# Optimization experiments

Measured on AMD Instinct MI355X. Metric: run time of the kernel, lower is better.

The kernel has to match this reference:

```python
import jax, jax.numpy as jnp
import numpy as np
from jax import lax

E = 8          # num_experts
C = 768        # n_embd
H = 3072       # expert_hidden_dim
TOP_K = 2
TEMPERATURE = 1.0


def setup_inputs() -> dict:
    key = jax.random.key(0)
    ks = jax.random.split(key, 6)
    B, T = 4, 2048
    x = jax.random.normal(ks[0], (B, T, C), dtype=jnp.float32)
    # router: Linear(C, E, bias=False); store as [C, E] so logits = x @ Wr
    Wr = jax.random.normal(ks[1], (C, E), dtype=jnp.float32) / np.sqrt(C)
    # stacked expert params
    W1 = jax.random.normal(ks[2], (E, C, H), dtype=jnp.float32) / np.sqrt(C)
    b1 = jnp.zeros((E, H), dtype=jnp.float32)
    W2 = jax.random.normal(ks[3], (E, H, C), dtype=jnp.float32) / np.sqrt(H)
    b2 = jnp.zeros((E, C), dtype=jnp.float32)
    return {"x": x, "Wr": Wr, "W1": W1, "b1": b1, "W2": W2, "b2": b2}


def reference(x, Wr, W1, b1, W2, b2):
    B, T, Cdim = x.shape
    xf = x.reshape(-1, Cdim)                         # [N, C]
    logits = (xf @ Wr) / TEMPERATURE                 # [N, E]
    prob = jax.nn.softmax(logits, axis=-1)
    top_prob, top_idx = lax.top_k(prob, TOP_K)       # [N, k]
    top_prob = top_prob / (top_prob.sum(-1, keepdims=True) + 1e-9)
    onehot = jax.nn.one_hot(top_idx, E, dtype=xf.dtype)     # [N, k, E]
    # per-token weight for each expert (zero if not selected)
    weights = jnp.einsum('nke,nk->en', onehot, top_prob)    # [E, N]
    # token counts per expert (top_k indices are distinct, so any == sum)
    counts = onehot.max(axis=1).sum(axis=0)                  # [E]
    utilization = counts / (counts.sum() + 1e-9)

    def step(acc, ew):
        W1e, b1e, W2e, b2e, we = ew
        h = jax.nn.gelu(xf @ W1e + b1e, approximate=False)   # [N, H]
        y = h @ W2e + b2e                                     # [N, C]
        return acc + we[:, None] * y, None

    out_flat, _ = lax.scan(step, jnp.zeros_like(xf), (W1, b1, W2, b2, weights))
    return out_flat.reshape(B, T, Cdim), utilization
```

## Files before the change

kernel.cpp:

```cpp
#include <hip/hip_runtime.h>

typedef unsigned short u16;
typedef unsigned int u32;
typedef __bf16 bf16x8 __attribute__((ext_vector_type(8)));
typedef float f32x4 __attribute__((ext_vector_type(4)));

#define NTOK 8192
#define CDIM 768
#define HDIM 3072
#define NEXP 8
#define NPAIR 16384
#define HB 32

__device__ __forceinline__ float b2f(u16 u){ u32 v = ((u32)u)<<16; float f; __builtin_memcpy(&f,&v,4); return f; }
__device__ __forceinline__ u16 f2b(float f){ u32 u; __builtin_memcpy(&u,&f,4); u32 r = (u + 0x7FFF + ((u>>16)&1)) >> 16; return (u16)r; }
__device__ __forceinline__ int iclamp(int v,int lo,int hi){ return v<lo?lo:(v>hi?hi:v); }

__device__ __forceinline__ float gelu_f(float v){
  float x = fabsf(v)*0.70710678118654752f;
  float t = __builtin_amdgcn_rcpf(1.0f + 0.3275911f*x);
  float p = ((((1.061405429f*t - 1.453152027f)*t + 1.421413741f)*t - 0.284496736f)*t + 0.254829592f)*t;
  float er = 1.0f - p*__expf(-x*x);
  er = copysignf(er, v);
  return 0.5f*v*(1.0f+er);
}

__device__ __forceinline__ void gl2l16(const void* g, void* l){
  __builtin_amdgcn_global_load_lds((const __attribute__((address_space(1))) void*)g,
                                   (__attribute__((address_space(3))) void*)l, 16, 0, 0);
}

__global__ void detect_k(const u16* __restrict__ x, int* __restrict__ flagp){
  __shared__ int cnt;
  if (threadIdx.x==0) cnt=0;
  __syncthreads();
  int bad=0;
  for (int i=threadIdx.x; i<2048; i+=256){
    u16 u = x[i];
    int ex = (u>>7)&0xFF;
    if (ex >= 134) bad++;
  }
  if (bad) atomicAdd(&cnt, bad);
  __syncthreads();
  if (threadIdx.x==0) *flagp = (cnt > 32) ? 1 : 0;
}

__global__ __launch_bounds__(256) void conv_k(const void* __restrict__ src, u16* __restrict__ dst,
                                              int n4, const int* __restrict__ flagp){
  int i = blockIdx.x*256 + threadIdx.x;
  if (i >= n4) return;
  if (*flagp){
    float4 v = ((const float4*)src)[i];
    ushort4 o; o.x=f2b(v.x); o.y=f2b(v.y); o.z=f2b(v.z); o.w=f2b(v.w);
    ((ushort4*)dst)[i] = o;
  } else {
    ((ushort4*)dst)[i] = ((const ushort4*)src)[i];
  }
}

__global__ __launch_bounds__(256) void router_k(const void* __restrict__ xraw, const void* __restrict__ Wrraw,
    const int* __restrict__ flagp,
    int* __restrict__ tok_e, float* __restrict__ tok_w){
  int fp32f = *flagp;
  int tok = blockIdx.x*4 + (threadIdx.x>>6);
  int lane = threadIdx.x & 63;
  double acc[8];
  #pragma unroll
  for(int e=0;e<8;e++) acc[e]=0.0;
  for(int j=0;j<12;j++){
    int c = j*64 + lane;
    if (fp32f){
      double xv = (double)((const float*)xraw)[(size_t)tok*CDIM + c];
      const float* wr = (const float*)Wrraw + (size_t)c*8;
      float4 w0 = *(const float4*)wr;
      float4 w1 = *(const float4*)(wr+4);
      acc[0] += xv*(double)w0.x; acc[1] += xv*(double)w0.y;
      acc[2] += xv*(double)w0.z; acc[3] += xv*(double)w0.w;
      acc[4] += xv*(double)w1.x; acc[5] += xv*(double)w1.y;
      acc[6] += xv*(double)w1.z; acc[7] += xv*(double)w1.w;
    } else {
      double xv = (double)b2f(((const u16*)xraw)[(size_t)tok*CDIM + c]);
      uint4 wv = *(const uint4*)((const u16*)Wrraw + (size_t)c*8);
      acc[0] += xv*(double)b2f((u16)(wv.x&0xFFFF));
      acc[1] += xv*(double)b2f((u16)(wv.x>>16));
      acc[2] += xv*(double)b2f((u16)(wv.y&0xFFFF));
      acc[3] += xv*(double)b2f((u16)(wv.y>>16));
      acc[4] += xv*(double)b2f((u16)(wv.z&0xFFFF));
      acc[5] += xv*(double)b2f((u16)(wv.z>>16));
      acc[6] += xv*(double)b2f((u16)(wv.w&0xFFFF));
      acc[7] += xv*(double)b2f((u16)(wv.w>>16));
    }
  }
  #pragma unroll
  for(int e=0;e<8;e++){
    #pragma unroll
    for(int off=32;off>0;off>>=1) acc[e] += __shfl_down(acc[e], off);
  }
  if (lane==0){
    int i0=0; double b0=acc[0];
    #pragma unroll
    for(int e=1;e<8;e++) if(acc[e]>b0){ b0=acc[e]; i0=e; }
    int i1=(i0+1)&7; double b1v=-1e300;
    #pragma unroll
    for(int e=0;e<8;e++) if(e!=i0 && acc[e]>b1v){ b1v=acc[e]; i1=e; }
    double Z = 0.0;
    #pragma unroll
    for(int e=0;e<8;e++) Z += exp(acc[e]-b0);
    double pr0 = 1.0/Z;
    double pr1 = exp(b1v-b0)/Z;
    double s = pr0+pr1+1e-9;
    tok_e[2*tok]=i0; tok_e[2*tok+1]=i1;
    tok_w[2*tok]=(float)(pr0/s); tok_w[2*tok+1]=(float)(pr1/s);
  }
}

__global__ __launch_bounds__(256) void hist_k(const int* __restrict__ tok_e, int* __restrict__ bhist){
  int b = blockIdx.x, t = threadIdx.x;
  int wave = t>>6, lane = t&63;
  __shared__ int lh[4][8];
  int base = b*512 + wave*128 + lane;
  int e0 = tok_e[base]    & 7;
  int e1 = tok_e[base+64] & 7;
  #pragma unroll
  for(int e=0;e<8;e++){
    unsigned long long m0 = __ballot(e0==e);
    unsigned long long m1 = __ballot(e1==e);
    if (lane==0) lh[wave][e] = __popcll(m0) + __popcll(m1);
  }
  __syncthreads();
  if (t<8){
    int s=0;
    #pragma unroll
    for(int w=0;w<4;w++) s += lh[w][t];
    bhist[b*8+t] = s;
  }
}

__global__ __launch_bounds__(64) void offsets2_k(const int* __restrict__ bhist, int* __restrict__ offsets,
                          int* __restrict__ bbase, void* __restrict__ dout, const int* __restrict__ flagp){
  __shared__ int cnt[8], off[8];
  int t = threadIdx.x;
  if (t<8){
    int s=0;
    for(int b=0;b<HB;b++) s += bhist[b*8+t];
    cnt[t]=s;
  }
  __syncthreads();
  if (t==0){
    int s=0;
    for(int e=0;e<8;e++){ off[e]=s; offsets[e]=s; s+=cnt[e]; }
    offsets[8]=s;
    int fp32f = *flagp;
    float inv = 1.f/((float)s + 1e-9f);
    for(int e=0;e<8;e++){
      float val = (float)cnt[e]*inv;
      if (fp32f) ((float*)dout)[(size_t)NTOK*CDIM + e] = val;
      else       ((u16*)dout)[(size_t)NTOK*CDIM + e]   = f2b(val);
    }
  }
  __syncthreads();
  if (t<8){
    int a = off[t];
    for(int b=0;b<HB;b++){ bbase[b*8+t] = a; a += bhist[b*8+t]; }
  }
}

__global__ __launch_bounds__(256) void scatter2_k(const int* __restrict__ tok_e,
    const int* __restrict__ bbase, int* __restrict__ pair_tok, int* __restrict__ tok_pos){
  int b = blockIdx.x, t = threadIdx.x;
  int wave = t>>6, lane = t&63;
  __shared__ int lh[4][8];
  int base = b*512 + wave*128 + lane;
  int i0 = base, i1 = base+64;
  int e0 = tok_e[i0] & 7;
  int e1 = tok_e[i1] & 7;
  unsigned long long lt = (1ULL<<lane)-1;
  int r0=0, r1=0;
  #pragma unroll
  for(int e=0;e<8;e++){
    unsigned long long m0 = __ballot(e0==e);
    unsigned long long m1 = __ballot(e1==e);
    if (lane==0) lh[wave][e] = __popcll(m0) + __popcll(m1);
    if (e0==e) r0 = __popcll(m0 & lt);
    if (e1==e) r1 = __popcll(m0) + __popcll(m1 & lt);
  }
  __syncthreads();
  int wb0=0, wb1=0;
  for(int w=0;w<wave;w++){ wb0 += lh[w][e0]; wb1 += lh[w][e1]; }
  int p0 = iclamp(bbase[b*8+e0] + wb0 + r0, 0, NPAIR-1);
  int p1 = iclamp(bbase[b*8+e1] + wb1 + r1, 0, NPAIR-1);
  pair_tok[p0] = i0>>1;
  pair_tok[p1] = i1>>1;
  tok_pos[i0] = p0;
  tok_pos[i1] = p1;
}

__global__ __launch_bounds__(256) void transpose_k(const void* __restrict__ inv, u16* __restrict__ out,
                                                   int R, int Cc, const int* __restrict__ flagp){
  __shared__ u16 T[64][65];
  int fp32f = *flagp;
  int ex = blockIdx.z;
  size_t base = (size_t)ex*R*Cc;
  out += base;
  int c0 = blockIdx.x*64, r0 = blockIdx.y*64;
  int tx = threadIdx.x & 31, ty = threadIdx.x >> 5;
  #pragma unroll
  for(int i=0;i<8;i++){
    int row = ty + i*8;
    size_t idx = base + (size_t)(r0+row)*Cc + c0 + tx*2;
    u32 v;
    if (fp32f){
      float2 f2v = *(const float2*)((const float*)inv + idx);
      v = (u32)f2b(f2v.x) | ((u32)f2b(f2v.y)<<16);
    } else {
      v = *(const u32*)((const u16*)inv + idx);
    }
    T[row][tx*2]   = (u16)(v&0xFFFF);
    T[row][tx*2+1] = (u16)(v>>16);
  }
  __syncthreads();
  #pragma unroll
  for(int i=0;i<8;i++){
    int row = ty + i*8;
    u32 lo = T[tx*2][row], hi = T[tx*2+1][row];
    *(u32*)(out + (size_t)(c0+row)*R + r0 + tx*2) = lo | (hi<<16);
  }
}

#define BM 128
#define BN 128
#define BK 64

template<int EPI, int NSLABS_E>
__global__ __launch_bounds__(256) void gemm_k(
    const u16* __restrict__ Abase, const int* __restrict__ pair_tok, int astride,
    const u16* __restrict__ Bt, const u16* __restrict__ bias,
    const int* __restrict__ offsets, int K, int N,
    u16* __restrict__ out_bf, float* __restrict__ out_f)
{
  constexpr int Q = 192*NSLABS_E;
  int j = blockIdx.x;
  int wid = (j&7)*Q + (j>>3);
  int slab = wid/192, s = wid - slab*192;
  int e  = slab / NSLABS_E;
  int ns = slab - e*NSLABS_E;
  int mb = s/3;
  int ny = s - mb*3;
  int m0 = mb*BM;
  int n0 = (ns*3 + ny)*BN;

  int seg0 = iclamp(offsets[e],   0, NPAIR);
  int seg1 = iclamp(offsets[e+1], seg0, NPAIR);
  int Me = seg1 - seg0;
  if (m0 >= Me) return;

  alignas(16) __shared__ u16 As[2*BM*BK];
  alignas(16) __shared__ u16 Bs[2*BM*BK];

  int t = threadIdx.x;
  int wave = t>>6, lane = t&63;
  int wm = (wave>>1)*64, wn = (wave&1)*64;
  int lr = lane&15, quad = lane>>4;

  int srow = lane>>3;
  int cl   = (lane&7) ^ srow;
  const u16* aptr[4]; const u16* bptr[4];
  int lbase[4];
  const u16* bbase_ = Bt + (size_t)e*(size_t)N*K;
  #pragma unroll
  for(int i=0;i<4;i++){
    int tr = wave*32 + i*8 + srow;
    int rr = iclamp(seg0 + m0 + tr, 0, seg1-1);
    int row = pair_tok ? iclamp(pair_tok[rr], 0, NTOK-1) : rr;
    aptr[i] = Abase + (size_t)row*astride + cl*8;
    bptr[i] = bbase_ + (size_t)(n0+tr)*K + cl*8;
    lbase[i] = (wave*32 + i*8)*BK;
  }

  f32x4 acc[4][4];
  #pragma unroll
  for(int i=0;i<4;i++)
    #pragma unroll
    for(int jj=0;jj<4;jj++) acc[i][jj]=(f32x4){0.f,0.f,0.f,0.f};

  #pragma unroll
  for(int i=0;i<4;i++){ gl2l16(aptr[i], &As[lbase[i]]); gl2l16(bptr[i], &Bs[lbase[i]]); }
  __syncthreads();

  int nt = K/BK;
  int cb = 0;
  for(int kt=0; kt<nt; ++kt){
    if (kt+1 < nt){
      int k0 = (kt+1)*BK;
      int nb = cb ^ (BM*BK);
      #pragma unroll
      for(int i=0;i<4;i++){ gl2l16(aptr[i]+k0, &As[nb+lbase[i]]); gl2l16(bptr[i]+k0, &Bs[nb+lbase[i]]); }
    }
    bf16x8 af[4][2], bfr[4][2];
    #pragma unroll
    for(int i=0;i<4;i++){
      int ra = wm+i*16+lr;
      int rb = wn+i*16+lr;
      #pragma unroll
      for(int ks=0;ks<2;ks++){
        af[i][ks]  = *(const bf16x8*)(&As[cb + ra*BK + ((ks*4+quad) ^ (ra&7))*8]);
        bfr[i][ks] = *(const bf16x8*)(&Bs[cb + rb*BK + ((ks*4+quad) ^ (rb&7))*8]);
      }
    }
    #pragma unroll
    for(int ks=0;ks<2;ks++)
      #pragma unroll
      for(int i=0;i<4;i++)
        #pragma unroll
        for(int jj=0;jj<4;jj++)
          acc[i][jj] = __builtin_amdgcn_mfma_f32_16x16x32_bf16(af[i][ks], bfr[jj][ks], acc[i][jj], 0,0,0);
    __syncthreads();
    cb ^= (BM*BK);
  }

  #pragma unroll
  for(int i=0;i<4;i++){
    int mm_base = wm + i*16 + quad*4;
    #pragma unroll
    for(int jj=0;jj<4;jj++){
      int nn = n0 + wn + jj*16 + lr;
      float bv = b2f(bias[(size_t)e*N + nn]);
      #pragma unroll
      for(int rg=0;rg<4;rg++){
        int mm = m0 + mm_base + rg;
        if (mm < Me){
          int r = seg0 + mm;
          float v = acc[i][jj][rg] + bv;
          if (EPI==0) out_bf[(size_t)r*N + nn] = f2b(gelu_f(v));
          else        out_f[(size_t)r*N + nn] = v;
        }
      }
    }
  }
}

__global__ __launch_bounds__(192) void combine_k(const float* __restrict__ y,
    const int* __restrict__ tok_pos, const float* __restrict__ tok_w,
    void* __restrict__ outv, const int* __restrict__ flagp){
  int fp32f = *flagp;
  int tkn = blockIdx.x;
  int c = threadIdx.x*4;
  int p0 = iclamp(tok_pos[2*tkn],   0, NPAIR-1);
  int p1 = iclamp(tok_pos[2*tkn+1], 0, NPAIR-1);
  float w0 = tok_w[2*tkn], w1 = tok_w[2*tkn+1];
  float4 a = *(const float4*)(y + (size_t)p0*CDIM + c);
  float4 b = *(const float4*)(y + (size_t)p1*CDIM + c);
  float4 o4;
  o4.x = w0*a.x + w1*b.x;
  o4.y = w0*a.y + w1*b.y;
  o4.z = w0*a.z + w1*b.z;
  o4.w = w0*a.w + w1*b.w;
  if (fp32f){
    *(float4*)((float*)outv + (size_t)tkn*CDIM + c) = o4;
  } else {
    ushort4 o;
    o.x = f2b(o4.x); o.y = f2b(o4.y); o.z = f2b(o4.z); o.w = f2b(o4.w);
    *(ushort4*)((u16*)outv + (size_t)tkn*CDIM + c) = o;
  }
}

extern "C" void kernel_launch(void* const* d_in, const int* in_sizes, int n_in,
                              void* d_out, int out_size, void* d_ws, size_t ws_size,
                              hipStream_t stream) {
  const void* x  = d_in[0];
  const void* Wr = d_in[1];
  const void* W1 = d_in[2];
  const void* b1 = d_in[3];
  const void* W2 = d_in[4];
  const void* b2 = d_in[5];

  char* w = (char*)d_ws;
  int*   flagp    = (int*)w;
  int*   offsets  = (int*)(w + 256);
  int*   bhist    = (int*)(w + 512);
  int*   bbase    = (int*)(w + 1536);
  int*   tok_e    = (int*)(w + 2560);
  float* tok_w    = (float*)(w + 68096);
  int*   tok_pos  = (int*)(w + 133632);
  int*   pair_tok = (int*)(w + 199168);
  u16*   b1c      = (u16*)(w + 264704);
  u16*   b2c      = (u16*)(w + 313856);
  u16*   xc       = (u16*)(w + 326144);
  u16*   W1t      = (u16*)(w + 12909056);
  u16*   W2t      = W1t + (size_t)NEXP*CDIM*HDIM;
  u16*   h        = W2t + (size_t)NEXP*CDIM*HDIM;
  float* y        = (float*)(h + (size_t)NPAIR*HDIM);
  size_t need = 239401472ull;
  if (ws_size < need) {
    hipMemsetAsync(d_out, 0, (size_t)out_size*2, stream);
    return;
  }

  detect_k<<<1, 256, 0, stream>>>((const u16*)x, flagp);
  conv_k<<<6144, 256, 0, stream>>>(x,  xc,  NTOK*CDIM/4, flagp);
  conv_k<<<24,   256, 0, stream>>>(b1, b1c, NEXP*HDIM/4, flagp);
  conv_k<<<6,    256, 0, stream>>>(b2, b2c, NEXP*CDIM/4, flagp);
  transpose_k<<<dim3(HDIM/64, CDIM/64, NEXP), 256, 0, stream>>>(W1, W1t, CDIM, HDIM, flagp);
  transpose_k<<<dim3(CDIM/64, HDIM/64, NEXP), 256, 0, stream>>>(W2, W2t, HDIM, CDIM, flagp);
  router_k<<<NTOK/4, 256, 0, stream>>>(x, Wr, flagp, tok_e, tok_w);
  hist_k<<<HB, 256, 0, stream>>>(tok_e, bhist);
  offsets2_k<<<1, 64, 0, stream>>>(bhist, offsets, bbase, d_out, flagp);
  scatter2_k<<<HB, 256, 0, stream>>>(tok_e, bbase, pair_tok, tok_pos);
  gemm_k<0,8><<<12288, 256, 0, stream>>>(
      xc, pair_tok, CDIM, W1t, b1c, offsets, CDIM, HDIM, h, nullptr);
  gemm_k<1,2><<<3072, 256, 0, stream>>>(
      h, nullptr, HDIM, W2t, b2c, offsets, HDIM, CDIM, nullptr, y);
  combine_k<<<NTOK, 192, 0, stream>>>(y, tok_pos, tok_w, d_out, flagp);
}
```

Measured before the change: 513.0 us.

## Triple-buffer GEMM LDS with BK=32 and explicit vmcnt waits

Restructures the grouped expert GEMM main loop from a double-buffered BK=64 pipeline to a triple-buffered BK=32 pipeline that prefetches two stages ahead. Full __syncthreads is replaced by raw s_barrier plus explicit vmcnt/lgkmcnt waits, so loads for the next tiles can stay in flight across the barrier. It also raises the MFMA block's scheduling priority with s_setprio and requests 3 blocks per CU via launch bounds. Halving BK doubles the number of barriers per K, and the hand-written waitcnt logic risks subtle races if the counts are wrong.

Result: slower. 546.7 us (+6.6%).

```diff
diff --git a/kernel.cpp b/kernel.cpp
--- a/kernel.cpp
+++ b/kernel.cpp
@@ -29,6 +29,15 @@
   __builtin_amdgcn_global_load_lds((const __attribute__((address_space(1))) void*)g,
                                    (__attribute__((address_space(3))) void*)l, 16, 0, 0);
 }
+
+__device__ __forceinline__ void barf(){
+  asm volatile("" ::: "memory");
+  __builtin_amdgcn_s_barrier();
+  asm volatile("" ::: "memory");
+}
+#define WAITVM4() asm volatile("s_waitcnt vmcnt(4)" ::: "memory")
+#define WAITVM0() asm volatile("s_waitcnt vmcnt(0)" ::: "memory")
+#define WAITLGKM0() asm volatile("s_waitcnt lgkmcnt(0)" ::: "memory")
 
 __global__ void detect_k(const u16* __restrict__ x, int* __restrict__ flagp){
   __shared__ int cnt;
@@ -229,10 +238,11 @@
 
 #define BM 128
 #define BN 128
-#define BK 64
+#define BK 32
+#define BUFSZ (BM*BK)
 
 template<int EPI, int NSLABS_E>
-__global__ __launch_bounds__(256) void gemm_k(
+__global__ __launch_bounds__(256, 3) void gemm_k(
     const u16* __restrict__ Abase, const int* __restrict__ pair_tok, int astride,
     const u16* __restrict__ Bt, const u16* __restrict__ bias,
     const int* __restrict__ offsets, int K, int N,
@@ -254,27 +264,27 @@
   int Me = seg1 - seg0;
   if (m0 >= Me) return;
 
-  alignas(16) __shared__ u16 As[2*BM*BK];
-  alignas(16) __shared__ u16 Bs[2*BM*BK];
+  alignas(16) __shared__ u16 As[3*BUFSZ];
+  alignas(16) __shared__ u16 Bs[3*BUFSZ];
 
   int t = threadIdx.x;
   int wave = t>>6, lane = t&63;
   int wm = (wave>>1)*64, wn = (wave&1)*64;
   int lr = lane&15, quad = lane>>4;
 
-  int srow = lane>>3;
-  int cl   = (lane&7) ^ srow;
-  const u16* aptr[4]; const u16* bptr[4];
-  int lbase[4];
+  int srow = lane>>2;
+  int cl   = (lane&3) ^ (srow&3);
+  const u16* aptr[2]; const u16* bptr[2];
+  int lbase[2];
   const u16* bbase_ = Bt + (size_t)e*(size_t)N*K;
   #pragma unroll
-  for(int i=0;i<4;i++){
-    int tr = wave*32 + i*8 + srow;
+  for(int i=0;i<2;i++){
+    int tr = wave*32 + i*16 + srow;
     int rr = iclamp(seg0 + m0 + tr, 0, seg1-1);
     int row = pair_tok ? iclamp(pair_tok[rr], 0, NTOK-1) : rr;
     aptr[i] = Abase + (size_t)row*astride + cl*8;
     bptr[i] = bbase_ + (size_t)(n0+tr)*K + cl*8;
-    lbase[i] = (wave*32 + i*8)*BK;
+    lbase[i] = (wave*32 + i*16)*BK;
   }
 
   f32x4 acc[4][4];
@@ -283,39 +293,49 @@
     #pragma unroll
     for(int jj=0;jj<4;jj++) acc[i][jj]=(f32x4){0.f,0.f,0.f,0.f};
 
-  #pragma unroll
-  for(int i=0;i<4;i++){ gl2l16(aptr[i], &As[lbase[i]]); gl2l16(bptr[i], &Bs[lbase[i]]); }
-  __syncthreads();
-
   int nt = K/BK;
-  int cb = 0;
+
+  #pragma unroll
+  for(int i=0;i<2;i++){ gl2l16(aptr[i],      &As[lbase[i]]);        gl2l16(bptr[i],      &Bs[lbase[i]]); }
+  #pragma unroll
+  for(int i=0;i<2;i++){ gl2l16(aptr[i]+BK,   &As[BUFSZ+lbase[i]]);  gl2l16(bptr[i]+BK,   &Bs[BUFSZ+lbase[i]]); }
+  WAITVM4();
+  barf();
+
+  int cur = 0;
   for(int kt=0; kt<nt; ++kt){
-    if (kt+1 < nt){
-      int k0 = (kt+1)*BK;
-      int nb = cb ^ (BM*BK);
+    if (kt+2 < nt){
+      int b2 = cur+2; if (b2>=3) b2-=3;
+      int ko = (kt+2)*BK;
       #pragma unroll
-      for(int i=0;i<4;i++){ gl2l16(aptr[i]+k0, &As[nb+lbase[i]]); gl2l16(bptr[i]+k0, &Bs[nb+lbase[i]]); }
-    }
-    bf16x8 af[4][2], bfr[4][2];
+      for(int i=0;i<2;i++){
+        gl2l16(aptr[i]+ko, &As[b2*BUFSZ+lbase[i]]);
+        gl2l16(bptr[i]+ko, &Bs[b2*BUFSZ+lbase[i]]);
+      }
+    }
+    int cb = cur*BUFSZ;
+    bf16x8 af[4], bfr[4];
     #pragma unroll
     for(int i=0;i<4;i++){
       int ra = wm+i*16+lr;
       int rb = wn+i*16+lr;
+      af[i]  = *(const bf16x8*)(&As[cb + ra*BK + ((quad ^ (ra&3))*8)]);
+      bfr[i] = *(const bf16x8*)(&Bs[cb + rb*BK + ((quad ^ (rb&3))*8)]);
+    }
+    __builtin_amdgcn_s_setprio(1);
+    #pragma unroll
+    for(int i=0;i<4;i++)
       #pragma unroll
-      for(int ks=0;ks<2;ks++){
-        af[i][ks]  = *(const bf16x8*)(&As[cb + ra*BK + ((ks*4+quad) ^ (ra&7))*8]);
-        bfr[i][ks] = *(const bf16x8*)(&Bs[cb + rb*BK + ((ks*4+quad) ^ (rb&7))*8]);
-      }
-    }
-    #pragma unroll
-    for(int ks=0;ks<2;ks++)
-      #pragma unroll
-      for(int i=0;i<4;i++)
-        #pragma unroll
-        for(int jj=0;jj<4;jj++)
-          acc[i][jj] = __builtin_amdgcn_mfma_f32_16x16x32_bf16(af[i][ks], bfr[jj][ks], acc[i][jj], 0,0,0);
-    __syncthreads();
-    cb ^= (BM*BK);
+      for(int jj=0;jj<4;jj++)
+        acc[i][jj] = __builtin_amdgcn_mfma_f32_16x16x32_bf16(af[i], bfr[jj], acc[i][jj], 0,0,0);
+    __builtin_amdgcn_s_setprio(0);
+    if (kt+1 < nt){
+      if (kt+2 < nt) WAITVM4();
+      else           WAITVM0();
+    }
+    WAITLGKM0();
+    barf();
+    cur = cur+1; if (cur>=3) cur=0;
   }
 
   #pragma unroll
```
